# Optimization experiments

Hardware: AMD Instinct MI355X
Metric: run time of the kernel (lower is better)

Reference implementation:

```python
import jax, jax.numpy as jnp
import numpy as np
from jax.ops import segment_sum

N_NODES = 100000
N_EDGES = 3200000
IN_DIM = 128
HID = 128
INT_DIM = 512
OUT_DIM = 3


def gcn_conv(x, W, b, src, dst, n):
    # PyG GCNConv (eval): add self-loops, symmetric normalization, aggregate, bias.
    loop = jnp.arange(n, dtype=src.dtype)
    s = jnp.concatenate([src, loop])
    d = jnp.concatenate([dst, loop])
    deg = segment_sum(jnp.ones_like(d, dtype=x.dtype), d, num_segments=n)  # [N]
    dinv = jnp.where(deg > 0, jax.lax.rsqrt(jnp.maximum(deg, 1e-12)), 0.0)
    norm = dinv[s] * dinv[d]                      # [E+N]
    h = x @ W                                      # [N, F_out]
    msg = h[s] * norm[:, None]                    # gather + scale
    return segment_sum(msg, d, num_segments=n) + b


def setup_inputs() -> dict:
    key = jax.random.key(0)
    ks = jax.random.split(key, 12)
    def lin(kw, kb, fi, fo):
        lim = 1.0 / np.sqrt(fi)
        W = jax.random.uniform(kw, (fi, fo), jnp.float32, -lim, lim)
        b = jax.random.uniform(kb, (fo,), jnp.float32, -lim, lim)
        return W, b
    x = jax.random.normal(ks[0], (N_NODES, IN_DIM), jnp.float32)
    edge_index = jax.random.randint(ks[1], (2, N_EDGES), 0, N_NODES, dtype=jnp.int64)
    W1, b1 = lin(ks[2], ks[3], IN_DIM, HID)
    W2, b2 = lin(ks[4], ks[5], HID, HID)
    W3, b3 = lin(ks[6], ks[7], HID, INT_DIM)
    Wi, bi = lin(ks[8], ks[9], INT_DIM, INT_DIM)
    Wc, bc = lin(ks[10], ks[11], INT_DIM, OUT_DIM)
    return {"x": x, "edge_index": edge_index, "W1": W1, "b1": b1, "W2": W2,
            "b2": b2, "W3": W3, "b3": b3, "Wi": Wi, "bi": bi, "Wc": Wc, "bc": bc}


def reference(x, edge_index, W1, b1, W2, b2, W3, b3, Wi, bi, Wc, bc):
    src, dst = edge_index[0], edge_index[1]
    n = x.shape[0]
    h = jax.nn.relu(gcn_conv(x, W1, b1, src, dst, n))
    h = jax.nn.relu(gcn_conv(h, W2, b2, src, dst, n))
    h = jax.nn.relu(gcn_conv(h, W3, b3, src, dst, n))
    h = jax.nn.relu(h @ Wi + bi)
    return h @ Wc + bc
```

## Files before the change

### kernel.cpp

```cpp
#include <hip/hip_runtime.h>
#include <hip/hip_fp16.h>

#define NN 100000
#define NE 3200000
#define NB 391
#define NBLK 512
#define EPB 6250

typedef unsigned int uint32;
typedef unsigned short u16;
typedef long long ll64;
typedef __attribute__((ext_vector_type(8))) _Float16 half8;
typedef __attribute__((ext_vector_type(4))) float f32x4;

__device__ inline float2 h2f2(uint32 u) {
  __half2 h = *reinterpret_cast<__half2*>(&u);
  return __half22float2(h);
}
__device__ inline uint32 f2h2(float x, float y) {
  return (uint32)__half_as_ushort(__float2half(x)) |
         ((uint32)__half_as_ushort(__float2half(y)) << 16);
}
__device__ inline int edge_at(const void* ei, int is64, ll64 idx) {
  return is64 ? (int)((const ll64*)ei)[idx] : ((const int*)ei)[idx];
}
__device__ inline int detect64(const int* ei32) {
  int acc = 0;
#pragma unroll
  for (int k = 1; k < 32; k += 2) acc |= ei32[k];
  return (acc == 0) ? 1 : 0;
}

__global__ __launch_bounds__(256) void k_binB(const void* __restrict__ ei,
                                              int* __restrict__ tbl) {
  __shared__ int h[NB];
  __shared__ int sIs64;
  int k = blockIdx.x, tid = threadIdx.x;
  for (int i = tid; i < NB; i += 256) h[i] = 0;
  if (tid == 0) sIs64 = detect64((const int*)ei);
  __syncthreads();
  int is64 = sIs64;
  ll64 beg = (ll64)k * EPB, end = beg + EPB;
  for (ll64 i = beg + tid; i < end; i += 256)
    atomicAdd(&h[edge_at(ei, is64, (ll64)NE + i) >> 8], 1);
  __syncthreads();
  for (int i = tid; i < NB; i += 256) tbl[k * NB + i] = h[i];
}
__global__ __launch_bounds__(512) void k_binC1(int* __restrict__ tbl,
                                               int* __restrict__ total) {
  __shared__ int sd[NBLK];
  int b = blockIdx.x, tid = threadIdx.x;
  int v = tbl[tid * NB + b];
  sd[tid] = v;
  __syncthreads();
  for (int off = 1; off < NBLK; off <<= 1) {
    int t = (tid >= off) ? sd[tid - off] : 0;
    __syncthreads();
    sd[tid] += t;
    __syncthreads();
  }
  tbl[tid * NB + b] = sd[tid] - v;
  if (tid == NBLK - 1) total[b] = sd[NBLK - 1];
}
__global__ __launch_bounds__(512) void k_binC2(const int* __restrict__ total,
                                               int* __restrict__ bbase,
                                               int* __restrict__ offs) {
  __shared__ int sd[512];
  int tid = threadIdx.x;
  int v = (tid < NB) ? total[tid] : 0;
  sd[tid] = v;
  __syncthreads();
  for (int off = 1; off < 512; off <<= 1) {
    int t = (tid >= off) ? sd[tid - off] : 0;
    __syncthreads();
    sd[tid] += t;
    __syncthreads();
  }
  if (tid < NB) bbase[tid] = sd[tid] - v;
  if (tid == 0) offs[NN] = NE;
}
__global__ __launch_bounds__(256) void k_binD(const void* __restrict__ ei,
                                              const int* __restrict__ tbl,
                                              const int* __restrict__ bbase,
                                              uint32* __restrict__ binned) {
  __shared__ int lb[NB];
  __shared__ int lc[NB];
  __shared__ int sIs64;
  int k = blockIdx.x, tid = threadIdx.x;
  for (int i = tid; i < NB; i += 256) {
    lb[i] = tbl[k * NB + i] + bbase[i];
    lc[i] = 0;
  }
  if (tid == 0) sIs64 = detect64((const int*)ei);
  __syncthreads();
  int is64 = sIs64;
  ll64 beg = (ll64)k * EPB, end = beg + EPB;
  for (ll64 i = beg + tid; i < end; i += 256) {
    int s = edge_at(ei, is64, i);
    int d = edge_at(ei, is64, (ll64)NE + i);
    int b = d >> 8;
    int r = atomicAdd(&lc[b], 1);
    binned[lb[b] + r] = (uint32)s | ((uint32)(d & 255) << 24);
  }
}
__global__ __launch_bounds__(256) void k_binE(const uint32* __restrict__ binned,
                                              const int* __restrict__ bbase,
                                              const int* __restrict__ total,
                                              int* __restrict__ offs,
                                              float* __restrict__ dinv,
                                              int* __restrict__ csr) {
  __shared__ int cnt[256], pref[256], fil[256];
  int b = blockIdx.x, tid = threadIdx.x;
  cnt[tid] = 0;
  fil[tid] = 0;
  __syncthreads();
  int base = bbase[b], tot = total[b];
  for (int i = tid; i < tot; i += 256) atomicAdd(&cnt[binned[base + i] >> 24], 1);
  __syncthreads();
  int v = cnt[tid];
  pref[tid] = v;
  __syncthreads();
  for (int off = 1; off < 256; off <<= 1) {
    int t = (tid >= off) ? pref[tid - off] : 0;
    __syncthreads();
    pref[tid] += t;
    __syncthreads();
  }
  int myoff = pref[tid] - v;
  pref[tid] = myoff;
  int node = b * 256 + tid;
  if (node < NN) {
    offs[node] = base + myoff;
    dinv[node] = rsqrtf((float)(v + 1));
  }
  __syncthreads();
  for (int i = tid; i < tot; i += 256) {
    uint32 w = binned[base + i];
    int dl = w >> 24;
    int r = atomicAdd(&fil[dl], 1);
    csr[base + pref[dl] + r] = (int)(w & 0xFFFFFFu);
  }
}

__device__ inline void packOne(const float* __restrict__ W, u16* __restrict__ ph,
                               int K, int N, int t) {
  int j = t & 7, lane = (t >> 3) & 63, tl = t >> 9;
  int kbn = K >> 5;
  int kb = tl % kbn, ntile = tl / kbn;
  int k = kb * 32 + (lane >> 4) * 8 + j;
  int n2 = ntile * 16 + (lane & 15);
  ph[t] = __half_as_ushort(__float2half(W[k * N + n2]));
}
__global__ void k_packhalf(const float* W1, const float* W2, const float* W3,
                           const float* Wi, u16* p1, u16* p2, u16* p3, u16* pi,
                           const float4* __restrict__ x, ushort4* __restrict__ xh,
                           const float* __restrict__ dinv) {
  int t = blockIdx.x * blockDim.x + threadIdx.x;
  if (t < 16384) packOne(W1, p1, 128, 128, t);
  else if (t < 32768) packOne(W2, p2, 128, 128, t - 16384);
  else if (t < 98304) packOne(W3, p3, 128, 512, t - 32768);
  else if (t < 360448) packOne(Wi, pi, 512, 512, t - 98304);
  else {
    int i = t - 360448;
    if (i < NN * 32) {
      float4 v = x[i];
      float sc = dinv[i >> 5];
      ushort4 o;
      o.x = __half_as_ushort(__float2half(v.x * sc));
      o.y = __half_as_ushort(__float2half(v.y * sc));
      o.z = __half_as_ushort(__float2half(v.z * sc));
      o.w = __half_as_ushort(__float2half(v.w * sc));
      xh[i] = o;
    }
  }
}

__global__ void k_agg(const uint32* __restrict__ xi, uint32* __restrict__ o,
                      const int* __restrict__ csr, const int* __restrict__ offs,
                      const float* __restrict__ dinv, int n) {
  int node = blockIdx.x * 4 + (threadIdx.x >> 6);
  int lane = threadIdx.x & 63;
  if (node >= n) return;
  int beg = offs[node], end = offs[node + 1];
  float ax = 0.f, ay = 0.f;
  int j = beg;
  for (; j + 7 < end; j += 8) {
    int s[8];
    float2 rr[8];
#pragma unroll
    for (int q = 0; q < 8; q++) s[q] = csr[j + q];
#pragma unroll
    for (int q = 0; q < 8; q++) rr[q] = h2f2(xi[(ll64)s[q] * 64 + lane]);
#pragma unroll
    for (int q = 0; q < 8; q++) {
      ax += rr[q].x;
      ay += rr[q].y;
    }
  }
  for (; j < end; j++) {
    float2 r = h2f2(xi[(ll64)csr[j] * 64 + lane]);
    ax += r.x;
    ay += r.y;
  }
  float di = dinv[node];
  float2 sf = h2f2(xi[(ll64)node * 64 + lane]);
  float vx = di * (ax + sf.x);
  float vy = di * (ay + sf.y);
  o[(ll64)node * 64 + lane] = f2h2(vx, vy);
}

__global__ __launch_bounds__(256, 4) void k_gemm_mfma(
    const u16* __restrict__ A, const u16* __restrict__ Bp,
    const float* __restrict__ bias, const float* __restrict__ dscale,
    u16* __restrict__ Co, int M, int N, int K) {
  int wave = threadIdx.x >> 6, lane = threadIdx.x & 63;
  int quad = lane >> 4, l16 = lane & 15;
  int row0 = blockIdx.x * 64, col0 = blockIdx.y * 64;
  int m = row0 + wave * 16 + l16;
  int mc = (m < M) ? m : (M - 1);
  int kbn = K >> 5;
  f32x4 acc[4] = {{0,0,0,0},{0,0,0,0},{0,0,0,0},{0,0,0,0}};
  const half8* Ar = (const half8*)&A[(ll64)mc * K];
  half8 ac = Ar[quad];
  half8 an = ac;
  half8 bc_[4], bn_[4];
#pragma unroll
  for (int nt = 0; nt < 4; nt++)
    bc_[nt] = *(const half8*)&Bp[((ll64)(((col0 >> 4) + nt) * kbn) * 64 + lane) * 8];
  for (int kb = 0; kb < kbn; kb++) {
    int kn = kb + 1;
    if (kn < kbn) {
      an = Ar[kn * 4 + quad];
#pragma unroll
      for (int nt = 0; nt < 4; nt++)
        bn_[nt] = *(const half8*)&Bp[((ll64)(((col0 >> 4) + nt) * kbn + kn) * 64 + lane) * 8];
    }
#pragma unroll
    for (int nt = 0; nt < 4; nt++)
      acc[nt] = __builtin_amdgcn_mfma_f32_16x16x32_f16(ac, bc_[nt], acc[nt], 0, 0, 0);
    ac = an;
#pragma unroll
    for (int nt = 0; nt < 4; nt++) bc_[nt] = bn_[nt];
  }
  float ds[4];
#pragma unroll
  for (int r = 0; r < 4; r++) {
    int rr = row0 + wave * 16 + quad * 4 + r;
    ds[r] = dscale[(rr < M) ? rr : (M - 1)];
  }
#pragma unroll
  for (int nt = 0; nt < 4; nt++) {
    int cc = col0 + nt * 16 + l16;
    float bv = bias[cc];
#pragma unroll
    for (int r = 0; r < 4; r++) {
      int rr = row0 + wave * 16 + quad * 4 + r;
      if (rr < M)
        Co[(ll64)rr * N + cc] =
            __half_as_ushort(__float2half(fmaxf(acc[nt][r] + bv, 0.0f) * ds[r]));
    }
  }
}

__global__ __launch_bounds__(256, 4) void k_tail32(
    const u16* __restrict__ a3, const u16* __restrict__ W3p,
    const float* __restrict__ b3, const u16* __restrict__ Wip,
    const float* __restrict__ bi, const float* __restrict__ Wc,
    const float* __restrict__ bc, float* __restrict__ out, int M) {
  __shared__ u16 h3s[32 * 512];
  __shared__ float sRed[4][32][3];
  int tid = threadIdx.x;
  int wave = tid >> 6, lane = tid & 63, quad = lane >> 4, l16 = lane & 15;
  int row0 = blockIdx.x * 32;

  half8 af[2][4];
#pragma unroll
  for (int rt = 0; rt < 2; rt++) {
    const half8* Ar = (const half8*)&a3[(ll64)(row0 + rt * 16 + l16) * 128];
#pragma unroll
    for (int kb = 0; kb < 4; kb++) af[rt][kb] = Ar[kb * 4 + quad];
  }
  {
    f32x4 acc0 = {0, 0, 0, 0}, acc1 = {0, 0, 0, 0};
    half8 bcur = *(const half8*)&W3p[((ll64)(wave * 32) * 64 + lane) * 8];
    half8 bnxt = bcur;
    for (int t = 0; t < 32; t++) {
      if (t + 1 < 32)
        bnxt = *(const half8*)&W3p[((ll64)(wave * 32 + t + 1) * 64 + lane) * 8];
      int kb = t & 3;
      acc0 = __builtin_amdgcn_mfma_f32_16x16x32_f16(af[0][kb], bcur, acc0, 0, 0, 0);
      acc1 = __builtin_amdgcn_mfma_f32_16x16x32_f16(af[1][kb], bcur, acc1, 0, 0, 0);
      if (kb == 3) {
        int nt = wave * 8 + (t >> 2);
        int col = nt * 16 + l16;
        float bv = b3[col];
#pragma unroll
        for (int r = 0; r < 4; r++) {
          int row0l = quad * 4 + r;
          float v0 = fmaxf(acc0[r] + bv, 0.0f);
          float v1 = fmaxf(acc1[r] + bv, 0.0f);
          int oct0 = (col >> 3) ^ (row0l & 7);
          h3s[row0l * 512 + oct0 * 8 + (col & 7)] = __half_as_ushort(__float2half(v0));
          int row1l = 16 + row0l;
          int oct1 = (col >> 3) ^ (row1l & 7);
          h3s[row1l * 512 + oct1 * 8 + (col & 7)] = __half_as_ushort(__float2half(v1));
        }
        acc0 = (f32x4){0, 0, 0, 0};
        acc1 = (f32x4){0, 0, 0, 0};
      }
      bcur = bnxt;
    }
  }
  __syncthreads();

  float acc3[2][4][3] = {};
  {
    f32x4 acc0 = {0, 0, 0, 0}, acc1 = {0, 0, 0, 0};
    half8 bcur = *(const half8*)&Wip[((ll64)(wave * 128) * 64 + lane) * 8];
    half8 bnxt = bcur;
    int r0l = l16, r1l = 16 + l16;
    int sw0 = r0l & 7;
    for (int t = 0; t < 128; t++) {
      if (t + 1 < 128)
        bnxt = *(const half8*)&Wip[((ll64)(wave * 128 + t + 1) * 64 + lane) * 8];
      int kb = t & 15;
      int oct = ((kb * 4 + quad) ^ sw0);
      half8 a0 = *(const half8*)&h3s[r0l * 512 + oct * 8];
      half8 a1 = *(const half8*)&h3s[r1l * 512 + oct * 8];
      acc0 = __builtin_amdgcn_mfma_f32_16x16x32_f16(a0, bcur, acc0, 0, 0, 0);
      acc1 = __builtin_amdgcn_mfma_f32_16x16x32_f16(a1, bcur, acc1, 0, 0, 0);
      if (kb == 15) {
        int nt = wave * 8 + (t >> 4);
        int col = nt * 16 + l16;
        float bv = bi[col];
        float w0 = Wc[col * 3 + 0], w1 = Wc[col * 3 + 1], w2 = Wc[col * 3 + 2];
#pragma unroll
        for (int r = 0; r < 4; r++) {
          float v0 = fmaxf(acc0[r] + bv, 0.0f);
          float v1 = fmaxf(acc1[r] + bv, 0.0f);
          acc3[0][r][0] += v0 * w0; acc3[0][r][1] += v0 * w1; acc3[0][r][2] += v0 * w2;
          acc3[1][r][0] += v1 * w0; acc3[1][r][1] += v1 * w1; acc3[1][r][2] += v1 * w2;
        }
        acc0 = (f32x4){0, 0, 0, 0};
        acc1 = (f32x4){0, 0, 0, 0};
      }
      bcur = bnxt;
    }
  }
#pragma unroll
  for (int rt = 0; rt < 2; rt++)
#pragma unroll
    for (int r = 0; r < 4; r++)
#pragma unroll
      for (int c = 0; c < 3; c++) {
        float v = acc3[rt][r][c];
        v += __shfl_xor(v, 1);
        v += __shfl_xor(v, 2);
        v += __shfl_xor(v, 4);
        v += __shfl_xor(v, 8);
        acc3[rt][r][c] = v;
      }
  if (l16 == 0) {
#pragma unroll
    for (int rt = 0; rt < 2; rt++)
#pragma unroll
      for (int r = 0; r < 4; r++)
#pragma unroll
        for (int c = 0; c < 3; c++)
          sRed[wave][rt * 16 + quad * 4 + r][c] = acc3[rt][r][c];
  }
  __syncthreads();
  if (tid < 96) {
    int row = tid / 3, c = tid % 3;
    out[(ll64)(row0 + row) * 3 + c] = sRed[0][row][c] + sRed[1][row][c] +
                                      sRed[2][row][c] + sRed[3][row][c] + bc[c];
  }
}

extern "C" void kernel_launch(void* const* d_in, const int* in_sizes, int n_in,
                              void* d_out, int out_size, void* d_ws, size_t ws_size,
                              hipStream_t stream) {
  const float* x  = (const float*)d_in[0];
  const void*  ei = d_in[1];
  const float* W1 = (const float*)d_in[2];
  const float* b1 = (const float*)d_in[3];
  const float* W2 = (const float*)d_in[4];
  const float* b2 = (const float*)d_in[5];
  const float* W3 = (const float*)d_in[6];
  const float* b3 = (const float*)d_in[7];
  const float* Wi = (const float*)d_in[8];
  const float* bi = (const float*)d_in[9];
  const float* Wc = (const float*)d_in[10];
  const float* bc = (const float*)d_in[11];
  float* out = (float*)d_out;

  char* ws = (char*)d_ws;
  const ll64 KB = 1ll << 10, MB = 1ll << 20;
  float* dinv  = (float*)(ws + 0);
  int*   offs  = (int*)(ws + 512 * KB);
  int*   total = (int*)(ws + 1 * MB + 64 * KB);
  int*   bbase = (int*)(ws + 1 * MB + 128 * KB);
  int*   tbl   = (int*)(ws + 1 * MB + 192 * KB);
  uint32* binned = (uint32*)(ws + 2 * MB);
  int*   csr   = (int*)(ws + 15 * MB);
  u16* pW1 = (u16*)(ws + 28 * MB);
  u16* pW2 = (u16*)(ws + 28 * MB + 64 * KB);
  u16* pW3 = (u16*)(ws + 28 * MB + 128 * KB);
  u16* pWi = (u16*)(ws + 28 * MB + 512 * KB);
  u16* xh   = (u16*)(ws + 29 * MB);
  u16* bufA = (u16*)(ws + 55 * MB);
  u16* bufB = (u16*)(ws + 81 * MB);

  const int TB = 256;
  k_binB<<<NBLK, TB, 0, stream>>>(ei, tbl);
  k_binC1<<<NB, NBLK, 0, stream>>>(tbl, total);
  k_binC2<<<1, 512, 0, stream>>>(total, bbase, offs);
  k_binD<<<NBLK, TB, 0, stream>>>(ei, tbl, bbase, binned);
  k_binE<<<NB, TB, 0, stream>>>(binned, bbase, total, offs, dinv, csr);
  k_packhalf<<<(360448 + NN * 32 + TB - 1) / TB, TB, 0, stream>>>(
      W1, W2, W3, Wi, pW1, pW2, pW3, pWi, (const float4*)x, (ushort4*)xh, dinv);

  const int MBk = (NN + 63) / 64;
  int aggBlocks = (NN + 3) / 4;
  dim3 g128(MBk, 2);

  k_agg<<<aggBlocks, TB, 0, stream>>>((const uint32*)xh, (uint32*)bufA, csr, offs, dinv, NN);
  k_gemm_mfma<<<g128, TB, 0, stream>>>(bufA, pW1, b1, dinv, bufB, NN, 128, 128);
  k_agg<<<aggBlocks, TB, 0, stream>>>((const uint32*)bufB, (uint32*)bufA, csr, offs, dinv, NN);
  k_gemm_mfma<<<g128, TB, 0, stream>>>(bufA, pW2, b2, dinv, bufB, NN, 128, 128);
  k_agg<<<aggBlocks, TB, 0, stream>>>((const uint32*)bufB, (uint32*)bufA, csr, offs, dinv, NN);
  k_tail32<<<NN / 32, TB, 0, stream>>>(bufA, pW3, b3, pWi, bi, Wc, bc, out, NN);
}
```

Baseline: 716.0 us.

## Use 16-byte gathers in aggregation and deepen weight prefetch in tail kernel

The aggregation kernel now handles four nodes per wavefront. Each 16-lane group gathers a 256-byte fp16 row with uint4 loads instead of 64 lanes doing 4-byte loads, which should cut the number of memory instructions and improve per-node parallelism. The edge unroll drops from 8 to 4 per group, but with four nodes per wave there are still more loads in flight. Separately, the tail kernel's weight streaming moves from a single-step lookahead to a 4-slot ring buffer prefetching three steps ahead. That buffer costs extra registers and may reduce occupancy.

```diff
diff --git a/kernel.cpp b/kernel.cpp
--- a/kernel.cpp
+++ b/kernel.cpp
@@ -178,35 +178,45 @@
 __global__ void k_agg(const uint32* __restrict__ xi, uint32* __restrict__ o,
                       const int* __restrict__ csr, const int* __restrict__ offs,
                       const float* __restrict__ dinv, int n) {
-  int node = blockIdx.x * 4 + (threadIdx.x >> 6);
-  int lane = threadIdx.x & 63;
+  int tid = threadIdx.x;
+  int lane = tid & 63;
+  int sub = lane >> 4, fl = lane & 15;
+  int node = blockIdx.x * 16 + (tid >> 6) * 4 + sub;
   if (node >= n) return;
   int beg = offs[node], end = offs[node + 1];
-  float ax = 0.f, ay = 0.f;
+  const uint4* xv = (const uint4*)xi;
+  float acc[8] = {};
   int j = beg;
-  for (; j + 7 < end; j += 8) {
-    int s[8];
-    float2 rr[8];
-#pragma unroll
-    for (int q = 0; q < 8; q++) s[q] = csr[j + q];
-#pragma unroll
-    for (int q = 0; q < 8; q++) rr[q] = h2f2(xi[(ll64)s[q] * 64 + lane]);
-#pragma unroll
-    for (int q = 0; q < 8; q++) {
-      ax += rr[q].x;
-      ay += rr[q].y;
+  for (; j + 3 < end; j += 4) {
+    int s[4];
+    uint4 r[4];
+#pragma unroll
+    for (int q = 0; q < 4; q++) s[q] = csr[j + q];
+#pragma unroll
+    for (int q = 0; q < 4; q++) r[q] = xv[(ll64)s[q] * 16 + fl];
+#pragma unroll
+    for (int q = 0; q < 4; q++) {
+      float2 p0 = h2f2(r[q].x), p1 = h2f2(r[q].y);
+      float2 p2 = h2f2(r[q].z), p3 = h2f2(r[q].w);
+      acc[0] += p0.x; acc[1] += p0.y; acc[2] += p1.x; acc[3] += p1.y;
+      acc[4] += p2.x; acc[5] += p2.y; acc[6] += p3.x; acc[7] += p3.y;
     }
   }
   for (; j < end; j++) {
-    float2 r = h2f2(xi[(ll64)csr[j] * 64 + lane]);
-    ax += r.x;
-    ay += r.y;
+    uint4 r = xv[(ll64)csr[j] * 16 + fl];
+    float2 p0 = h2f2(r.x), p1 = h2f2(r.y), p2 = h2f2(r.z), p3 = h2f2(r.w);
+    acc[0] += p0.x; acc[1] += p0.y; acc[2] += p1.x; acc[3] += p1.y;
+    acc[4] += p2.x; acc[5] += p2.y; acc[6] += p3.x; acc[7] += p3.y;
   }
   float di = dinv[node];
-  float2 sf = h2f2(xi[(ll64)node * 64 + lane]);
-  float vx = di * (ax + sf.x);
-  float vy = di * (ay + sf.y);
-  o[(ll64)node * 64 + lane] = f2h2(vx, vy);
+  uint4 sf = xv[(ll64)node * 16 + fl];
+  float2 q0 = h2f2(sf.x), q1 = h2f2(sf.y), q2 = h2f2(sf.z), q3 = h2f2(sf.w);
+  uint4 ov;
+  ov.x = f2h2(di * (acc[0] + q0.x), di * (acc[1] + q0.y));
+  ov.y = f2h2(di * (acc[2] + q1.x), di * (acc[3] + q1.y));
+  ov.z = f2h2(di * (acc[4] + q2.x), di * (acc[5] + q2.y));
+  ov.w = f2h2(di * (acc[6] + q3.x), di * (acc[7] + q3.y));
+  ((uint4*)o)[(ll64)node * 16 + fl] = ov;
 }
 
 __global__ __launch_bounds__(256, 4) void k_gemm_mfma(
@@ -282,11 +292,15 @@
   }
   {
     f32x4 acc0 = {0, 0, 0, 0}, acc1 = {0, 0, 0, 0};
-    half8 bcur = *(const half8*)&W3p[((ll64)(wave * 32) * 64 + lane) * 8];
-    half8 bnxt = bcur;
+    half8 bq[4];
+#pragma unroll
+    for (int p = 0; p < 3; p++)
+      bq[p] = *(const half8*)&W3p[((ll64)(wave * 32 + p) * 64 + lane) * 8];
+#pragma unroll 4
     for (int t = 0; t < 32; t++) {
-      if (t + 1 < 32)
-        bnxt = *(const half8*)&W3p[((ll64)(wave * 32 + t + 1) * 64 + lane) * 8];
+      if (t + 3 < 32)
+        bq[(t + 3) & 3] = *(const half8*)&W3p[((ll64)(wave * 32 + t + 3) * 64 + lane) * 8];
+      half8 bcur = bq[t & 3];
       int kb = t & 3;
       acc0 = __builtin_amdgcn_mfma_f32_16x16x32_f16(af[0][kb], bcur, acc0, 0, 0, 0);
       acc1 = __builtin_amdgcn_mfma_f32_16x16x32_f16(af[1][kb], bcur, acc1, 0, 0, 0);
@@ -308,7 +322,6 @@
         acc0 = (f32x4){0, 0, 0, 0};
         acc1 = (f32x4){0, 0, 0, 0};
       }
-      bcur = bnxt;
     }
   }
   __syncthreads();
@@ -316,13 +329,17 @@
   float acc3[2][4][3] = {};
   {
     f32x4 acc0 = {0, 0, 0, 0}, acc1 = {0, 0, 0, 0};
-    half8 bcur = *(const half8*)&Wip[((ll64)(wave * 128) * 64 + lane) * 8];
-    half8 bnxt = bcur;
+    half8 bq[4];
+#pragma unroll
+    for (int p = 0; p < 3; p++)
+      bq[p] = *(const half8*)&Wip[((ll64)(wave * 128 + p) * 64 + lane) * 8];
     int r0l = l16, r1l = 16 + l16;
     int sw0 = r0l & 7;
+#pragma unroll 4
     for (int t = 0; t < 128; t++) {
-      if (t + 1 < 128)
-        bnxt = *(const half8*)&Wip[((ll64)(wave * 128 + t + 1) * 64 + lane) * 8];
+      if (t + 3 < 128)
+        bq[(t + 3) & 3] = *(const half8*)&Wip[((ll64)(wave * 128 + t + 3) * 64 + lane) * 8];
+      half8 bcur = bq[t & 3];
       int kb = t & 15;
       int oct = ((kb * 4 + quad) ^ sw0);
       half8 a0 = *(const half8*)&h3s[r0l * 512 + oct * 8];
@@ -344,7 +361,6 @@
         acc0 = (f32x4){0, 0, 0, 0};
         acc1 = (f32x4){0, 0, 0, 0};
       }
-      bcur = bnxt;
     }
   }
 #pragma unroll
@@ -421,7 +437,7 @@
       W1, W2, W3, Wi, pW1, pW2, pW3, pWi, (const float4*)x, (ushort4*)xh, dinv);
 
   const int MBk = (NN + 63) / 64;
-  int aggBlocks = (NN + 3) / 4;
+  int aggBlocks = (NN + 15) / 16;
   dim3 g128(MBk, 2);
 
   k_agg<<<aggBlocks, TB, 0, stream>>>((const uint32*)xh, (uint32*)bufA, csr, offs, dinv, NN);
```

Measured after the change: 698.4 us. -2.5%, faster.
